# Optimization experiments

Measured on AMD Instinct MI355X. Metric: run time of the kernel, lower is better.

## Reference

```python
import jax, jax.numpy as jnp
import numpy as np

NT, NRV, NR = 100000, 200000, 300000  # tile / road_vertex / road node counts
E = 400000                             # edges per edge type
B, H, P, A = 64, 128, 64, 512          # graphs, hidden, player_state_dim, action_dim


def _gat(h_src, h_dst, src, dst, W, a_s, a_d, b, n_dst):
    # PyG GATConv, heads=1, shared lin for src/dst, no self loops (bipartite)
    hs = h_src @ W                      # [Ns, H]
    hd = h_dst @ W                      # [Nd, H]
    e = jax.nn.leaky_relu((hs @ a_s)[src] + (hd @ a_d)[dst], 0.2)  # [E]
    m = jax.ops.segment_max(e, dst, num_segments=n_dst)
    w = jnp.exp(e - m[dst])
    denom = jax.ops.segment_sum(w, dst, num_segments=n_dst)
    alpha = w / jnp.maximum(denom[dst], 1e-16)                      # segment softmax
    out = jax.ops.segment_sum(alpha[:, None] * hs[src], dst, num_segments=n_dst)
    return out + b


def _mean_pool(x, batch, nb):
    s = jax.ops.segment_sum(x, batch, num_segments=nb)
    c = jax.ops.segment_sum(jnp.ones((x.shape[0],), x.dtype), batch, num_segments=nb)
    return s / jnp.maximum(c, 1.0)[:, None]


def setup_inputs():
    ks = iter(jax.random.split(jax.random.key(0), 64))
    f32 = jnp.float32

    def lin(i, o):
        return (jax.random.normal(next(ks), (i, o), f32) / np.float32(np.sqrt(i)))

    d = {}
    d['x_tile'] = jax.random.normal(next(ks), (NT, 8), f32)
    d['x_rv'] = jax.random.normal(next(ks), (NRV, 13), f32)
    d['x_road'] = jax.random.normal(next(ks), (NR, 4), f32)
    d['x_player'] = jax.random.normal(next(ks), (B, P), f32)
    # node encoders
    d['enc_t_W'] = lin(8, H);  d['enc_t_b'] = jnp.zeros((H,), f32)
    d['enc_rv_W'] = lin(13, H); d['enc_rv_b'] = jnp.zeros((H,), f32)
    d['enc_r_W'] = lin(4, H);  d['enc_r_b'] = jnp.zeros((H,), f32)
    # six GAT convs
    for name in ['rv2t', 't2rv', 'r2rv', 'rv2r', 't2r', 'r2t']:
        d[name + '_W'] = lin(H, H)
        d[name + '_as'] = jax.random.normal(next(ks), (H,), f32) * 0.1
        d[name + '_ad'] = jax.random.normal(next(ks), (H,), f32) * 0.1
        d[name + '_b'] = jnp.zeros((H,), f32)
    # player MLP + output head (input: 3H pooled + H player)
    d['fc1_W'] = lin(P, H); d['fc1_b'] = jnp.zeros((H,), f32)
    d['fc2_W'] = lin(H, H); d['fc2_b'] = jnp.zeros((H,), f32)
    d['out_W'] = lin(4 * H, A); d['out_b'] = jnp.zeros((A,), f32)
    # edges (src bounded by source-type count, dst by dest-type count)
    ri = lambda n, hi: jax.random.randint(n, (E,), 0, hi, jnp.int32)
    d['e_rv2t_src'] = ri(next(ks), NRV); d['e_rv2t_dst'] = ri(next(ks), NT)
    d['e_t2rv_src'] = ri(next(ks), NT);  d['e_t2rv_dst'] = ri(next(ks), NRV)
    d['e_r2rv_src'] = ri(next(ks), NR);  d['e_r2rv_dst'] = ri(next(ks), NRV)
    d['e_rv2r_src'] = ri(next(ks), NRV); d['e_rv2r_dst'] = ri(next(ks), NR)
    d['e_t2r_src'] = ri(next(ks), NT);   d['e_t2r_dst'] = ri(next(ks), NR)
    d['e_r2t_src'] = ri(next(ks), NR);   d['e_r2t_dst'] = ri(next(ks), NT)
    # batch assignment per node type
    d['batch_tile'] = jnp.sort(jax.random.randint(next(ks), (NT,), 0, B, jnp.int32))
    d['batch_rv'] = jnp.sort(jax.random.randint(next(ks), (NRV,), 0, B, jnp.int32))
    d['batch_road'] = jnp.sort(jax.random.randint(next(ks), (NR,), 0, B, jnp.int32))
    return d


def reference(x_tile, x_rv, x_road, x_player,
              enc_t_W, enc_t_b, enc_rv_W, enc_rv_b, enc_r_W, enc_r_b,
              rv2t_W, rv2t_as, rv2t_ad, rv2t_b,
              t2rv_W, t2rv_as, t2rv_ad, t2rv_b,
              r2rv_W, r2rv_as, r2rv_ad, r2rv_b,
              rv2r_W, rv2r_as, rv2r_ad, rv2r_b,
              t2r_W, t2r_as, t2r_ad, t2r_b,
              r2t_W, r2t_as, r2t_ad, r2t_b,
              fc1_W, fc1_b, fc2_W, fc2_b, out_W, out_b,
              e_rv2t_src, e_rv2t_dst, e_t2rv_src, e_t2rv_dst,
              e_r2rv_src, e_r2rv_dst, e_rv2r_src, e_rv2r_dst,
              e_t2r_src, e_t2r_dst, e_r2t_src, e_r2t_dst,
              batch_tile, batch_rv, batch_road):
    # node encoders
    h_t = x_tile @ enc_t_W + enc_t_b
    h_rv = x_rv @ enc_rv_W + enc_rv_b
    h_r = x_road @ enc_r_W + enc_r_b
    # hetero GAT, aggr='sum' over edge types per destination node type
    o_t = (_gat(h_rv, h_t, e_rv2t_src, e_rv2t_dst, rv2t_W, rv2t_as, rv2t_ad, rv2t_b, NT)
           + _gat(h_r, h_t, e_r2t_src, e_r2t_dst, r2t_W, r2t_as, r2t_ad, r2t_b, NT))
    o_rv = (_gat(h_t, h_rv, e_t2rv_src, e_t2rv_dst, t2rv_W, t2rv_as, t2rv_ad, t2rv_b, NRV)
            + _gat(h_r, h_rv, e_r2rv_src, e_r2rv_dst, r2rv_W, r2rv_as, r2rv_ad, r2rv_b, NRV))
    o_r = (_gat(h_rv, h_r, e_rv2r_src, e_rv2r_dst, rv2r_W, rv2r_as, rv2r_ad, rv2r_b, NR)
           + _gat(h_t, h_r, e_t2r_src, e_t2r_dst, t2r_W, t2r_as, t2r_ad, t2r_b, NR))
    # global mean pool per node type, concat -> [B, 3H]
    x_all = jnp.concatenate([_mean_pool(o_t, batch_tile, B),
                             _mean_pool(o_rv, batch_rv, B),
                             _mean_pool(o_r, batch_road, B)], axis=1)
    # player branch
    p = jax.nn.relu(x_player @ fc1_W + fc1_b)
    p = jax.nn.relu(p @ fc2_W + fc2_b)
    x = jnp.concatenate([x_all, p], axis=1)  # [B, 4H]
    return x @ out_W + out_b                 # [B, A]
```

## Files before the change

### kernel.cpp

```cpp
#include <hip/hip_runtime.h>


constexpr int kNT = 100000, kNRV = 200000, kNR = 300000, kE = 400000;
constexpr int kTOTE = 6 * kE;
constexpr int kSLOT = 1088;
constexpr int kPSZ  = 6 * kSLOT;
constexpr int kNB   = 367;

constexpr long long OFF_C    = 0;
constexpr long long OFF_VS   = 13056;
constexpr long long OFF_VD   = 13176;
constexpr long long OFF_P    = 13296;
constexpr long long OFF_XCAT = 19824;
constexpr long long OFF_LS   = 52592;
constexpr long long OFF_LD   = 1252592;
constexpr long long OFF_PB   = 52592;
constexpr long long OFF_W16  = 2452592;
constexpr long long OFF_DR2  = 3652592;
constexpr long long OFF_XR   = 6052592;

__constant__ const int kLSB[6] = {0, 200000, 300000, 600000, 800000, 900000};
__constant__ const int kDRB[6] = {0, 100000, 300000, 500000, 800000, 1100000};
__constant__ const int kDLEN[6] = {100000, 200000, 200000, 300000, 300000, 100000};

__global__ __launch_bounds__(256) void precompute_kernel(
    const float* encW_t, const float* encb_t,
    const float* encW_rv, const float* encb_rv,
    const float* encW_r, const float* encb_r,
    const float* W0, const float* as0, const float* ad0,
    const float* W1, const float* as1, const float* ad1,
    const float* W2, const float* as2, const float* ad2,
    const float* W3, const float* as3, const float* ad3,
    const float* W4, const float* as4, const float* ad4,
    const float* W5, const float* as5, const float* ad5,
    float* Cws, float* vsw, float* vdw)
{
  const float* encW[3] = {encW_t, encW_rv, encW_r};
  const float* encb[3] = {encb_t, encb_rv, encb_r};
  const int    Ks[3]   = {8, 13, 4};
  const float* Wv[6]  = {W0, W1, W2, W3, W4, W5};
  const float* asv[6] = {as0, as1, as2, as3, as4, as5};
  const float* adv[6] = {ad0, ad1, ad2, ad3, ad4, ad5};
  const int srcT[6] = {1, 0, 2, 1, 0, 2};
  const int dstT[6] = {0, 1, 1, 2, 2, 0};

  __shared__ float Cl[2176];
  __shared__ float wv[128];

  int et = blockIdx.x;
  int tid = threadIdx.x;
  int st = srcT[et], dt = dstT[et];
  const float* eW = encW[st];
  const float* eB = encb[st];
  int K = Ks[st];
  const float* W = Wv[et];
  const float* a_s = asv[et];
  const float* a_d = adv[et];
  float* Cslot = Cws + et * 2176;

  for (int idx = tid; idx < (K + 1) * 128; idx += 256) {
    int r = idx >> 7, j = idx & 127;
    const float* row = (r < K) ? (eW + r * 128) : eB;
    float acc = 0.f;
    for (int m = 0; m < 128; ++m) acc += row[m] * W[m * 128 + j];
    int o = (r < K) ? (r * 128 + j) : (2048 + j);
    Cl[o] = acc;
    Cslot[o] = acc;
  }
  if (tid < 128) {
    float acc = 0.f;
    for (int j = 0; j < 128; ++j) acc += W[tid * 128 + j] * a_d[j];
    wv[tid] = acc;
  }
  __syncthreads();
  if (tid <= K) {
    const float* row = (tid < K) ? (Cl + tid * 128) : (Cl + 2048);
    float acc = 0.f;
    for (int j = 0; j < 128; ++j) acc += row[j] * a_s[j];
    vsw[et * 20 + (tid < K ? tid : 16)] = acc;
  }
  int KD = Ks[dt];
  if (tid >= 32 && tid <= 32 + KD) {
    int k = tid - 32;
    const float* row = (k < KD) ? (encW[dt] + k * 128) : encb[dt];
    float acc = 0.f;
    for (int m = 0; m < 128; ++m) acc += row[m] * wv[m];
    vdw[et * 20 + (k < KD ? k : 16)] = acc;
  }
}

template <int K, int RH>
__device__ __forceinline__ void prep_one(
    const float* __restrict__ xr, float bf,
    const float* __restrict__ vsA, const float* __restrict__ vsB,
    const float* __restrict__ vdA, const float* __restrict__ vdB,
    float* lsA, float* lsB, float* ldA, float* ldB,
    float2* dr2A, float2* dr2B, _Float16* xrec)
{
  float a0 = 0.f, a1 = 0.f, a2 = 0.f, a3 = 0.f;
#pragma unroll
  for (int k = 0; k < K; ++k) {
    float xv = xr[k];
    a0 += xv * vsA[k]; a1 += xv * vsB[k];
    a2 += xv * vdA[k]; a3 += xv * vdB[k];
    xrec[k] = (_Float16)xv;
  }
#pragma unroll
  for (int k = K; k < RH; ++k) xrec[k] = (_Float16)0.f;
  *lsA = a0 + vsA[16];
  *lsB = a1 + vsB[16];
  *ldA = a2 + vdA[16];
  *ldB = a3 + vdB[16];
  *dr2A = make_float2(0.f, bf);
  *dr2B = make_float2(0.f, bf);
}

__global__ __launch_bounds__(256) void prep_kernel(
    const float* __restrict__ x_t, const float* __restrict__ x_rv,
    const float* __restrict__ x_r,
    const int* __restrict__ bt, const int* __restrict__ brv,
    const int* __restrict__ br,
    const float* __restrict__ vsw, const float* __restrict__ vdw,
    float* __restrict__ LS, float* __restrict__ LD,
    float2* __restrict__ DR2, _Float16* __restrict__ XR)
{
  int n = blockIdx.x * 256 + threadIdx.x;
  if (n >= kNT + kNRV + kNR) return;
  if (n < kNT) {
    prep_one<8, 8>(x_t + n * 8, (float)bt[n],
                   vsw + 1 * 20, vsw + 4 * 20, vdw + 0 * 20, vdw + 5 * 20,
                   LS + 200000 + n, LS + 800000 + n,
                   LD + 0 + n, LD + 1100000 + n,
                   DR2 + 0 + n, DR2 + 1100000 + n,
                   XR + (long long)n * 8);
  } else if (n < kNT + kNRV) {
    int m = n - kNT;
    prep_one<13, 16>(x_rv + m * 13, (float)brv[m],
                     vsw + 0 * 20, vsw + 3 * 20, vdw + 1 * 20, vdw + 2 * 20,
                     LS + 0 + m, LS + 600000 + m,
                     LD + 100000 + m, LD + 300000 + m,
                     DR2 + 100000 + m, DR2 + 300000 + m,
                     XR + 800000 + (long long)m * 16);
  } else {
    int m = n - kNT - kNRV;
    prep_one<4, 4>(x_r + m * 4, (float)br[m],
                   vsw + 2 * 20, vsw + 5 * 20, vdw + 3 * 20, vdw + 4 * 20,
                   LS + 300000 + m, LS + 900000 + m,
                   LD + 500000 + m, LD + 800000 + m,
                   DR2 + 500000 + m, DR2 + 800000 + m,
                   XR + 4000000 + (long long)m * 4);
  }
}

__global__ __launch_bounds__(256) void passA_kernel(
    const int* s0, const int* s1, const int* s2,
    const int* s3, const int* s4, const int* s5,
    const int* d0, const int* d1, const int* d2,
    const int* d3, const int* d4, const int* d5,
    const float* __restrict__ LS, const float* __restrict__ LD,
    float* __restrict__ DR2f, _Float16* __restrict__ W16)
{
  int i = blockIdx.x * 256 + threadIdx.x;
  if (i >= kTOTE) return;
  int et = i / kE;
  int e = i - et * kE;
  const int* sp; const int* dp;
  switch (et) {
    case 0: sp = s0; dp = d0; break;
    case 1: sp = s1; dp = d1; break;
    case 2: sp = s2; dp = d2; break;
    case 3: sp = s3; dp = d3; break;
    case 4: sp = s4; dp = d4; break;
    default: sp = s5; dp = d5; break;
  }
  int lsb = kLSB[et], drb = kDRB[et];
  int s = sp[e], d = dp[e];
  float t = LS[lsb + s] + LD[drb + d];
  t = t > 0.f ? t : 0.2f * t;
  _Float16 h = (_Float16)__expf(t);
  W16[i] = h;
  unsafeAtomicAdd(&DR2f[(long long)(drb + d) * 2], (float)h);
}

template <int K, int RH>
__device__ __forceinline__ void passB_loop(
    const int* __restrict__ sp, const int* __restrict__ dp,
    int drb, int dlen, long long xrb,
    const _Float16* __restrict__ W16et, const float2* __restrict__ DR2,
    const _Float16* __restrict__ XR, float* __restrict__ lp,
    int start, int stride)
{
  int nItems = kE + dlen;
  for (int i = start; i < nItems; i += stride) {
    if (i < kE) {
      int s = sp[i], d = dp[i];
      float2 rec = DR2[drb + d];
      float w = (float)W16et[i];
      float alpha = w / fmaxf(rec.x, 1e-16f);
      int b = (int)rec.y;
      const _Float16* xp = XR + xrb + (long long)s * RH;
      float xv[K];
      if constexpr (RH == 4) {
        union { uint2 u; _Float16 h[4]; } U;
        U.u = *(const uint2*)xp;
#pragma unroll
        for (int k = 0; k < K; ++k) xv[k] = (float)U.h[k];
      } else if constexpr (RH == 8) {
        union { uint4 u; _Float16 h[8]; } U;
        U.u = *(const uint4*)xp;
#pragma unroll
        for (int k = 0; k < K; ++k) xv[k] = (float)U.h[k];
      } else {
        union { uint4 u[2]; _Float16 h[16]; } U;
        U.u[0] = *(const uint4*)xp;
        U.u[1] = *(const uint4*)(xp + 8);
#pragma unroll
        for (int k = 0; k < K; ++k) xv[k] = (float)U.h[k];
      }
#pragma unroll
      for (int k = 0; k < K; ++k) atomicAdd(lp + k * 64 + b, alpha * xv[k]);
    } else {
      int j = i - kE;
      float2 rec = DR2[drb + j];
      if (rec.x > 0.f) atomicAdd(lp + 1024 + (int)rec.y, 1.f);
    }
  }
}

__global__ __launch_bounds__(256) void passB_kernel(
    const int* s0, const int* s1, const int* s2,
    const int* s3, const int* s4, const int* s5,
    const int* d0, const int* d1, const int* d2,
    const int* d3, const int* d4, const int* d5,
    const _Float16* __restrict__ W16, const float2* __restrict__ DR2,
    const _Float16* __restrict__ XR, float* __restrict__ PB)
{
  __shared__ float lp[kSLOT];
  for (int j = threadIdx.x; j < kSLOT; j += 256) lp[j] = 0.f;
  __syncthreads();
  int et  = blockIdx.x / kNB;
  int blk = blockIdx.x - et * kNB;
  int start = blk * 256 + threadIdx.x;
  int stride = kNB * 256;
  int drb = kDRB[et], dlen = kDLEN[et];
  const _Float16* W16et = W16 + (long long)et * kE;
  switch (et) {
    case 0: passB_loop<13,16>(s0, d0, drb, dlen, 800000,  W16et, DR2, XR, lp, start, stride); break;
    case 1: passB_loop< 8, 8>(s1, d1, drb, dlen, 0,       W16et, DR2, XR, lp, start, stride); break;
    case 2: passB_loop< 4, 4>(s2, d2, drb, dlen, 4000000, W16et, DR2, XR, lp, start, stride); break;
    case 3: passB_loop<13,16>(s3, d3, drb, dlen, 800000,  W16et, DR2, XR, lp, start, stride); break;
    case 4: passB_loop< 8, 8>(s4, d4, drb, dlen, 0,       W16et, DR2, XR, lp, start, stride); break;
    default: passB_loop<4, 4>(s5, d5, drb, dlen, 4000000, W16et, DR2, XR, lp, start, stride); break;
  }
  __syncthreads();
  float* dst = PB + (long long)blockIdx.x * kSLOT;
  for (int j = threadIdx.x; j < kSLOT; j += 256) dst[j] = lp[j];
}

__global__ __launch_bounds__(256) void reduceP_kernel(
    const float* __restrict__ PB, float* __restrict__ P)
{
  int j = blockIdx.x * 256 + threadIdx.x;
  if (j >= kPSZ) return;
  int et = j / kSLOT;
  int jj = j - et * kSLOT;
  const float* base = PB + (long long)et * kNB * kSLOT + jj;
  float s = 0.f;
  int b = 0;
  for (; b + 8 <= kNB; b += 8) {
    float v0 = base[(long long)(b + 0) * kSLOT];
    float v1 = base[(long long)(b + 1) * kSLOT];
    float v2 = base[(long long)(b + 2) * kSLOT];
    float v3 = base[(long long)(b + 3) * kSLOT];
    float v4 = base[(long long)(b + 4) * kSLOT];
    float v5 = base[(long long)(b + 5) * kSLOT];
    float v6 = base[(long long)(b + 6) * kSLOT];
    float v7 = base[(long long)(b + 7) * kSLOT];
    s += ((v0 + v1) + (v2 + v3)) + ((v4 + v5) + (v6 + v7));
  }
  for (; b < kNB; ++b) s += base[(long long)b * kSLOT];
  P[j] = s;
}

__device__ __forceinline__ int lowb(const int* a, int n, int v) {
  int lo = 0, hi = n;
  while (lo < hi) { int mid = (lo + hi) >> 1; if (a[mid] < v) lo = mid + 1; else hi = mid; }
  return lo;
}

__global__ __launch_bounds__(128) void finalize_kernel(
    const int* __restrict__ bt, const int* __restrict__ brv, const int* __restrict__ br,
    const float* __restrict__ xp,
    const float* __restrict__ fc1W, const float* __restrict__ fc1b,
    const float* __restrict__ fc2W, const float* __restrict__ fc2b,
    const float* __restrict__ b_rv2t, const float* __restrict__ b_r2t,
    const float* __restrict__ b_t2rv, const float* __restrict__ b_r2rv,
    const float* __restrict__ b_rv2r, const float* __restrict__ b_t2r,
    const float* __restrict__ Cws, const float* __restrict__ P,
    float* __restrict__ xcat)
{
  int b = blockIdx.x, tid = threadIdx.x;
  __shared__ float xps[64];
  __shared__ float p1s[128];
  __shared__ int cnts[3];
  if (tid < 64) xps[tid] = xp[b * 64 + tid];
  if (tid < 3) {
    const int* ba = (tid == 0) ? bt : (tid == 1 ? brv : br);
    int N = (tid == 0) ? kNT : (tid == 1 ? kNRV : kNR);
    cnts[tid] = lowb(ba, N, b + 1) - lowb(ba, N, b);
  }
  __syncthreads();
  float a = fc1b[tid];
  for (int k = 0; k < 64; ++k) a += xps[k] * fc1W[k * 128 + tid];
  p1s[tid] = fmaxf(a, 0.f);
  __syncthreads();
  float a2 = fc2b[tid];
  for (int k = 0; k < 128; ++k) a2 += p1s[k] * fc2W[k * 128 + tid];
  xcat[b * 512 + 384 + tid] = fmaxf(a2, 0.f);
  const int etA[3] = {0, 1, 3}, etB[3] = {5, 2, 4};
  const int KAv[3] = {13, 8, 13}, KBv[3] = {4, 4, 8};
  for (int t3 = 0; t3 < 3; ++t3) {
    int eA = etA[t3], eB = etB[t3];
    const float* CA = Cws + eA * 2176;
    const float* CB = Cws + eB * 2176;
    const float* pA = P + eA * kSLOT;
    const float* pB = P + eB * kSLOT;
    float cA = pA[1024 + b];
    float cB = pB[1024 + b];
    float v = cA * CA[2048 + tid] + cB * CB[2048 + tid];
    for (int k = 0; k < KAv[t3]; ++k) v += pA[k * 64 + b] * CA[k * 128 + tid];
    for (int k = 0; k < KBv[t3]; ++k) v += pB[k * 64 + b] * CB[k * 128 + tid];
    float cnt = (float)max(cnts[t3], 1);
    const float* bb1 = (t3 == 0) ? b_rv2t : (t3 == 1 ? b_t2rv : b_rv2r);
    const float* bb2 = (t3 == 0) ? b_r2t  : (t3 == 1 ? b_r2rv : b_t2r);
    xcat[b * 512 + t3 * 128 + tid] = v / cnt + bb1[tid] + bb2[tid];
  }
}

__global__ __launch_bounds__(256) void out_kernel(
    const float* __restrict__ xcat, const float* __restrict__ outW,
    const float* __restrict__ outb, float* __restrict__ out)
{
  int g = blockIdx.x * 256 + threadIdx.x;
  int r = g >> 9, c = g & 511;
  const float* xr = xcat + r * 512;
  float acc = outb[c];
  for (int k = 0; k < 512; ++k) acc += xr[k] * outW[k * 512 + c];
  out[g] = acc;
}

extern "C" void kernel_launch(void* const* d_in, const int* in_sizes, int n_in,
                              void* d_out, int out_size, void* d_ws, size_t ws_size,
                              hipStream_t stream) {
  const float* x_tile   = (const float*)d_in[0];
  const float* x_rv     = (const float*)d_in[1];
  const float* x_road   = (const float*)d_in[2];
  const float* x_player = (const float*)d_in[3];
  const float* enc_t_W  = (const float*)d_in[4];
  const float* enc_t_b  = (const float*)d_in[5];
  const float* enc_rv_W = (const float*)d_in[6];
  const float* enc_rv_b = (const float*)d_in[7];
  const float* enc_r_W  = (const float*)d_in[8];
  const float* enc_r_b  = (const float*)d_in[9];
  const float* W[6]; const float* As[6]; const float* Ad[6]; const float* Bb[6];
  for (int et = 0; et < 6; ++et) {
    W[et]  = (const float*)d_in[10 + 4 * et];
    As[et] = (const float*)d_in[11 + 4 * et];
    Ad[et] = (const float*)d_in[12 + 4 * et];
    Bb[et] = (const float*)d_in[13 + 4 * et];
  }
  const float* fc1W = (const float*)d_in[34];
  const float* fc1b = (const float*)d_in[35];
  const float* fc2W = (const float*)d_in[36];
  const float* fc2b = (const float*)d_in[37];
  const float* outW = (const float*)d_in[38];
  const float* outb = (const float*)d_in[39];
  const int* esrc[6]; const int* edst[6];
  for (int et = 0; et < 6; ++et) {
    esrc[et] = (const int*)d_in[40 + 2 * et];
    edst[et] = (const int*)d_in[41 + 2 * et];
  }
  const int* batch_t  = (const int*)d_in[52];
  const int* batch_rv = (const int*)d_in[53];
  const int* batch_r  = (const int*)d_in[54];

  float* wsF = (float*)d_ws;
  float* Cws  = wsF + OFF_C;
  float* vsw  = wsF + OFF_VS;
  float* vdw  = wsF + OFF_VD;
  float* P    = wsF + OFF_P;
  float* xcat = wsF + OFF_XCAT;
  float* LS   = wsF + OFF_LS;
  float* LD   = wsF + OFF_LD;
  float* PB   = wsF + OFF_PB;
  _Float16* W16 = (_Float16*)(wsF + OFF_W16);
  float2* DR2 = (float2*)(wsF + OFF_DR2);
  float* DR2f = wsF + OFF_DR2;
  _Float16* XR = (_Float16*)(wsF + OFF_XR);
  float* out  = (float*)d_out;

  precompute_kernel<<<6, 256, 0, stream>>>(
      enc_t_W, enc_t_b, enc_rv_W, enc_rv_b, enc_r_W, enc_r_b,
      W[0], As[0], Ad[0], W[1], As[1], Ad[1], W[2], As[2], Ad[2],
      W[3], As[3], Ad[3], W[4], As[4], Ad[4], W[5], As[5], Ad[5],
      Cws, vsw, vdw);

  prep_kernel<<<(kNT + kNRV + kNR + 255) / 256, 256, 0, stream>>>(
      x_tile, x_rv, x_road, batch_t, batch_rv, batch_r, vsw, vdw,
      LS, LD, DR2, XR);

  passA_kernel<<<(kTOTE + 255) / 256, 256, 0, stream>>>(
      esrc[0], esrc[1], esrc[2], esrc[3], esrc[4], esrc[5],
      edst[0], edst[1], edst[2], edst[3], edst[4], edst[5],
      LS, LD, DR2f, W16);

  passB_kernel<<<6 * kNB, 256, 0, stream>>>(
      esrc[0], esrc[1], esrc[2], esrc[3], esrc[4], esrc[5],
      edst[0], edst[1], edst[2], edst[3], edst[4], edst[5],
      W16, DR2, XR, PB);

  reduceP_kernel<<<(kPSZ + 255) / 256, 256, 0, stream>>>(PB, P);

  finalize_kernel<<<64, 128, 0, stream>>>(
      batch_t, batch_rv, batch_r, x_player,
      fc1W, fc1b, fc2W, fc2b,
      Bb[0], Bb[5], Bb[1], Bb[2], Bb[3], Bb[4],
      Cws, P, xcat);

  out_kernel<<<128, 256, 0, stream>>>(xcat, outW, outb, out);

  (void)in_sizes; (void)n_in; (void)out_size; (void)ws_size;
}
```

Measured before the change: 515.9 us.

## Map edge types to XCDs via blockIdx modulo 8 for L2 locality

Both passA and passB now launch a fixed grid of 2048 blocks. Blocks are routed by blockIdx&7, which assumes round-robin dispatch across the 8 XCDs, so each XCD works on a contiguous edge range or a single edge type. This is meant to keep the gathered LS/LD/DR2/XR data for one edge type in that XCD's L2 instead of spreading it across all of them. The degree-count loop in passB now does a wave-level segmented scan, so runs of nodes in the same graph produce one shared-memory atomic instead of one each. reduceP is rewritten for the new per-block layout, and it relies on the block-to-XCD mapping being as assumed.

After: 537.8 us. +4.3%, slower.

```diff
diff --git a/kernel.cpp b/kernel.cpp
--- a/kernel.cpp
+++ b/kernel.cpp
@@ -5,7 +5,7 @@
 constexpr int kTOTE = 6 * kE;
 constexpr int kSLOT = 1088;
 constexpr int kPSZ  = 6 * kSLOT;
-constexpr int kNB   = 367;
+constexpr int kGRID = 2048;
 
 constexpr long long OFF_C    = 0;
 constexpr long long OFF_VS   = 13056;
@@ -22,6 +22,12 @@
 __constant__ const int kLSB[6] = {0, 200000, 300000, 600000, 800000, 900000};
 __constant__ const int kDRB[6] = {0, 100000, 300000, 500000, 800000, 1100000};
 __constant__ const int kDLEN[6] = {100000, 200000, 200000, 300000, 300000, 100000};
+
+__constant__ const int kXCD2ET[8] = {0, 0, 1, 2, 3, 3, 4, 5};
+__constant__ const int kXCDSUB[8] = {0, 1, 0, 0, 0, 1, 0, 0};
+__constant__ const int kETNX[6]   = {2, 1, 1, 2, 1, 1};
+__constant__ const int kETXCDA[6] = {0, 2, 3, 4, 6, 7};
+__constant__ const int kETXCDB[6] = {1, 2, 3, 5, 6, 7};
 
 __global__ __launch_bounds__(256) void precompute_kernel(
     const float* encW_t, const float* encb_t,
@@ -152,19 +158,14 @@
   }
 }
 
-__global__ __launch_bounds__(256) void passA_kernel(
+__device__ __forceinline__ void pickSD(
+    int et,
     const int* s0, const int* s1, const int* s2,
     const int* s3, const int* s4, const int* s5,
     const int* d0, const int* d1, const int* d2,
     const int* d3, const int* d4, const int* d5,
-    const float* __restrict__ LS, const float* __restrict__ LD,
-    float* __restrict__ DR2f, _Float16* __restrict__ W16)
-{
-  int i = blockIdx.x * 256 + threadIdx.x;
-  if (i >= kTOTE) return;
-  int et = i / kE;
-  int e = i - et * kE;
-  const int* sp; const int* dp;
+    const int*& sp, const int*& dp)
+{
   switch (et) {
     case 0: sp = s0; dp = d0; break;
     case 1: sp = s1; dp = d1; break;
@@ -173,13 +174,46 @@
     case 4: sp = s4; dp = d4; break;
     default: sp = s5; dp = d5; break;
   }
-  int lsb = kLSB[et], drb = kDRB[et];
-  int s = sp[e], d = dp[e];
-  float t = LS[lsb + s] + LD[drb + d];
-  t = t > 0.f ? t : 0.2f * t;
-  _Float16 h = (_Float16)__expf(t);
-  W16[i] = h;
-  unsafeAtomicAdd(&DR2f[(long long)(drb + d) * 2], (float)h);
+}
+
+__global__ __launch_bounds__(256, 8) void passA_kernel(
+    const int* s0, const int* s1, const int* s2,
+    const int* s3, const int* s4, const int* s5,
+    const int* d0, const int* d1, const int* d2,
+    const int* d3, const int* d4, const int* d5,
+    const float* __restrict__ LS, const float* __restrict__ LD,
+    float* __restrict__ DR2f, _Float16* __restrict__ W16)
+{
+  int xcd  = blockIdx.x & 7;
+  int slot = blockIdx.x >> 3;
+  int c0 = xcd * (kTOTE / 8);
+  int c1 = c0 + (kTOTE / 8);
+  int etA = c0 / kE;
+  int eA1 = (etA + 1) * kE;
+  if (eA1 > c1) eA1 = c1;
+
+  for (int half = 0; half < 2; ++half) {
+    int et, rs, re;
+    if (half == 0) {
+      et = etA; rs = c0; re = eA1;
+    } else {
+      if (eA1 >= c1) break;
+      et = etA + 1; rs = eA1; re = c1;
+    }
+    const int* sp; const int* dp;
+    pickSD(et, s0, s1, s2, s3, s4, s5, d0, d1, d2, d3, d4, d5, sp, dp);
+    int lsb = kLSB[et], drb = kDRB[et];
+    int ebase = et * kE;
+    for (int i = rs + slot * 256 + (int)threadIdx.x; i < re; i += 65536) {
+      int e = i - ebase;
+      int s = sp[e], d = dp[e];
+      float t = LS[lsb + s] + LD[drb + d];
+      t = t > 0.f ? t : 0.2f * t;
+      _Float16 h = (_Float16)__expf(t);
+      W16[i] = h;
+      unsafeAtomicAdd(&DR2f[(long long)(drb + d) * 2], (float)h);
+    }
+  }
 }
 
 template <int K, int RH>
@@ -188,46 +222,59 @@
     int drb, int dlen, long long xrb,
     const _Float16* __restrict__ W16et, const float2* __restrict__ DR2,
     const _Float16* __restrict__ XR, float* __restrict__ lp,
-    int start, int stride)
-{
-  int nItems = kE + dlen;
-  for (int i = start; i < nItems; i += stride) {
-    if (i < kE) {
-      int s = sp[i], d = dp[i];
-      float2 rec = DR2[drb + d];
-      float w = (float)W16et[i];
-      float alpha = w / fmaxf(rec.x, 1e-16f);
-      int b = (int)rec.y;
-      const _Float16* xp = XR + xrb + (long long)s * RH;
-      float xv[K];
-      if constexpr (RH == 4) {
-        union { uint2 u; _Float16 h[4]; } U;
-        U.u = *(const uint2*)xp;
-#pragma unroll
-        for (int k = 0; k < K; ++k) xv[k] = (float)U.h[k];
-      } else if constexpr (RH == 8) {
-        union { uint4 u; _Float16 h[8]; } U;
-        U.u = *(const uint4*)xp;
-#pragma unroll
-        for (int k = 0; k < K; ++k) xv[k] = (float)U.h[k];
-      } else {
-        union { uint4 u[2]; _Float16 h[16]; } U;
-        U.u[0] = *(const uint4*)xp;
-        U.u[1] = *(const uint4*)(xp + 8);
-#pragma unroll
-        for (int k = 0; k < K; ++k) xv[k] = (float)U.h[k];
-      }
-#pragma unroll
-      for (int k = 0; k < K; ++k) atomicAdd(lp + k * 64 + b, alpha * xv[k]);
+    int bIdx, int stride)
+{
+  int tid = threadIdx.x;
+  int lane = tid & 63;
+
+  for (int i = bIdx * 256 + tid; i < kE; i += stride) {
+    int s = sp[i], d = dp[i];
+    float2 rec = DR2[drb + d];
+    float w = (float)W16et[i];
+    float alpha = w / fmaxf(rec.x, 1e-16f);
+    int b = (int)rec.y;
+    const _Float16* xp = XR + xrb + (long long)s * RH;
+    float xv[K];
+    if constexpr (RH == 4) {
+      union { uint2 u; _Float16 h[4]; } U;
+      U.u = *(const uint2*)xp;
+#pragma unroll
+      for (int k = 0; k < K; ++k) xv[k] = (float)U.h[k];
+    } else if constexpr (RH == 8) {
+      union { uint4 u; _Float16 h[8]; } U;
+      U.u = *(const uint4*)xp;
+#pragma unroll
+      for (int k = 0; k < K; ++k) xv[k] = (float)U.h[k];
     } else {
-      int j = i - kE;
-      float2 rec = DR2[drb + j];
-      if (rec.x > 0.f) atomicAdd(lp + 1024 + (int)rec.y, 1.f);
+      union { uint4 u[2]; _Float16 h[16]; } U;
+      U.u[0] = *(const uint4*)xp;
+      U.u[1] = *(const uint4*)(xp + 8);
+#pragma unroll
+      for (int k = 0; k < K; ++k) xv[k] = (float)U.h[k];
     }
-  }
-}
-
-__global__ __launch_bounds__(256) void passB_kernel(
+#pragma unroll
+    for (int k = 0; k < K; ++k) atomicAdd(lp + k * 64 + b, alpha * xv[k]);
+  }
+
+  for (int base = bIdx * 256 + (tid & ~63); base < dlen; base += stride) {
+    int j = base + lane;
+    bool act = j < dlen;
+    float2 rec = act ? DR2[drb + j] : make_float2(0.f, 0.f);
+    int b = act ? (int)rec.y : (64 + lane);
+    int v = (act && rec.x > 0.f) ? 1 : 0;
+#pragma unroll
+    for (int d2 = 1; d2 < 64; d2 <<= 1) {
+      int ob = __shfl_up(b, d2);
+      int ov = __shfl_up(v, d2);
+      if (lane >= d2 && ob == b) v += ov;
+    }
+    int bn = __shfl_down(b, 1);
+    bool tailq = (lane == 63) || (bn != b);
+    if (tailq && v > 0) atomicAdd(lp + 1024 + b, (float)v);
+  }
+}
+
+__global__ __launch_bounds__(256, 8) void passB_kernel(
     const int* s0, const int* s1, const int* s2,
     const int* s3, const int* s4, const int* s5,
     const int* d0, const int* d1, const int* d2,
@@ -238,19 +285,21 @@
   __shared__ float lp[kSLOT];
   for (int j = threadIdx.x; j < kSLOT; j += 256) lp[j] = 0.f;
   __syncthreads();
-  int et  = blockIdx.x / kNB;
-  int blk = blockIdx.x - et * kNB;
-  int start = blk * 256 + threadIdx.x;
-  int stride = kNB * 256;
+  int xcd  = blockIdx.x & 7;
+  int slot = blockIdx.x >> 3;
+  int et = kXCD2ET[xcd];
+  int nx = kETNX[et];
+  int bIdx = slot * nx + kXCDSUB[xcd];
+  int stride = 65536 * nx;
   int drb = kDRB[et], dlen = kDLEN[et];
   const _Float16* W16et = W16 + (long long)et * kE;
   switch (et) {
-    case 0: passB_loop<13,16>(s0, d0, drb, dlen, 800000,  W16et, DR2, XR, lp, start, stride); break;
-    case 1: passB_loop< 8, 8>(s1, d1, drb, dlen, 0,       W16et, DR2, XR, lp, start, stride); break;
-    case 2: passB_loop< 4, 4>(s2, d2, drb, dlen, 4000000, W16et, DR2, XR, lp, start, stride); break;
-    case 3: passB_loop<13,16>(s3, d3, drb, dlen, 800000,  W16et, DR2, XR, lp, start, stride); break;
-    case 4: passB_loop< 8, 8>(s4, d4, drb, dlen, 0,       W16et, DR2, XR, lp, start, stride); break;
-    default: passB_loop<4, 4>(s5, d5, drb, dlen, 4000000, W16et, DR2, XR, lp, start, stride); break;
+    case 0: passB_loop<13,16>(s0, d0, drb, dlen, 800000,  W16et, DR2, XR, lp, bIdx, stride); break;
+    case 1: passB_loop< 8, 8>(s1, d1, drb, dlen, 0,       W16et, DR2, XR, lp, bIdx, stride); break;
+    case 2: passB_loop< 4, 4>(s2, d2, drb, dlen, 4000000, W16et, DR2, XR, lp, bIdx, stride); break;
+    case 3: passB_loop<13,16>(s3, d3, drb, dlen, 800000,  W16et, DR2, XR, lp, bIdx, stride); break;
+    case 4: passB_loop< 8, 8>(s4, d4, drb, dlen, 0,       W16et, DR2, XR, lp, bIdx, stride); break;
+    default: passB_loop<4, 4>(s5, d5, drb, dlen, 4000000, W16et, DR2, XR, lp, bIdx, stride); break;
   }
   __syncthreads();
   float* dst = PB + (long long)blockIdx.x * kSLOT;
@@ -264,21 +313,19 @@
   if (j >= kPSZ) return;
   int et = j / kSLOT;
   int jj = j - et * kSLOT;
-  const float* base = PB + (long long)et * kNB * kSLOT + jj;
   float s = 0.f;
-  int b = 0;
-  for (; b + 8 <= kNB; b += 8) {
-    float v0 = base[(long long)(b + 0) * kSLOT];
-    float v1 = base[(long long)(b + 1) * kSLOT];
-    float v2 = base[(long long)(b + 2) * kSLOT];
-    float v3 = base[(long long)(b + 3) * kSLOT];
-    float v4 = base[(long long)(b + 4) * kSLOT];
-    float v5 = base[(long long)(b + 5) * kSLOT];
-    float v6 = base[(long long)(b + 6) * kSLOT];
-    float v7 = base[(long long)(b + 7) * kSLOT];
-    s += ((v0 + v1) + (v2 + v3)) + ((v4 + v5) + (v6 + v7));
-  }
-  for (; b < kNB; ++b) s += base[(long long)b * kSLOT];
+  {
+    const float* base = PB + (long long)kETXCDA[et] * kSLOT + jj;
+#pragma unroll 8
+    for (int slot = 0; slot < 256; ++slot)
+      s += base[(long long)slot * (8 * kSLOT)];
+  }
+  if (kETNX[et] == 2) {
+    const float* base = PB + (long long)kETXCDB[et] * kSLOT + jj;
+#pragma unroll 8
+    for (int slot = 0; slot < 256; ++slot)
+      s += base[(long long)slot * (8 * kSLOT)];
+  }
   P[j] = s;
 }
 
@@ -409,12 +456,12 @@
       x_tile, x_rv, x_road, batch_t, batch_rv, batch_r, vsw, vdw,
       LS, LD, DR2, XR);
 
-  passA_kernel<<<(kTOTE + 255) / 256, 256, 0, stream>>>(
+  passA_kernel<<<kGRID, 256, 0, stream>>>(
       esrc[0], esrc[1], esrc[2], esrc[3], esrc[4], esrc[5],
       edst[0], edst[1], edst[2], edst[3], edst[4], edst[5],
       LS, LD, DR2f, W16);
 
-  passB_kernel<<<6 * kNB, 256, 0, stream>>>(
+  passB_kernel<<<kGRID, 256, 0, stream>>>(
       esrc[0], esrc[1], esrc[2], esrc[3], esrc[4], esrc[5],
       edst[0], edst[1], edst[2], edst[3], edst[4], edst[5],
       W16, DR2, XR, PB);
```

## Pack per-node features with logits, recompute edge weights, and reduce partials atomically

Applied to the files above, without the earlier changes.

Each source node now gets one packed record holding its fp16 features and its source-side attention logits, so a single vector load serves both. The destination logit and the graph id are packed into one float by storing the batch index in the low mantissa bits. The fp16 edge-weight buffer is dropped: edge weights are recomputed in the second pass instead of stored. Each thread handles five edges to raise memory-level parallelism. Node counts are reduced with a wave-level segmented scan, and per-block partial sums go into 8 slabs via atomics instead of a full per-block partial array. The trade-offs are extra exp work, slightly perturbed logits from the mantissa embedding, and atomic contention on the slabs.

After: 527.0 us. 2.1% more time.

```diff
diff --git a/kernel.cpp b/kernel.cpp
--- a/kernel.cpp
+++ b/kernel.cpp
@@ -2,26 +2,44 @@
 
 
 constexpr int kNT = 100000, kNRV = 200000, kNR = 300000, kE = 400000;
-constexpr int kTOTE = 6 * kE;
 constexpr int kSLOT = 1088;
 constexpr int kPSZ  = 6 * kSLOT;
-constexpr int kNB   = 367;
+constexpr int kNBE  = 342;
+constexpr int kNTH  = kNBE * 256;
+constexpr int kEPT  = 5;
 
 constexpr long long OFF_C    = 0;
 constexpr long long OFF_VS   = 13056;
 constexpr long long OFF_VD   = 13176;
 constexpr long long OFF_P    = 13296;
 constexpr long long OFF_XCAT = 19824;
-constexpr long long OFF_LS   = 52592;
-constexpr long long OFF_LD   = 1252592;
-constexpr long long OFF_PB   = 52592;
-constexpr long long OFF_W16  = 2452592;
-constexpr long long OFF_DR2  = 3652592;
-constexpr long long OFF_XR   = 6052592;
-
-__constant__ const int kLSB[6] = {0, 200000, 300000, 600000, 800000, 900000};
-__constant__ const int kDRB[6] = {0, 100000, 300000, 500000, 800000, 1100000};
-__constant__ const int kDLEN[6] = {100000, 200000, 200000, 300000, 300000, 100000};
+constexpr long long OFF_SRV  = 52592;
+constexpr long long OFF_ST   = 3252592;
+constexpr long long OFF_SR   = 4052592;
+constexpr long long OFF_LDD  = 5252592;
+constexpr long long OFF_P8   = 7652592;
+
+__constant__ const int kDRB[6]   = {0, 100000, 300000, 500000, 800000, 1100000};
+__constant__ const int kDLEN[6]  = {100000, 200000, 200000, 300000, 300000, 100000};
+__constant__ const int kLSOFF[6] = {7, 4, 2, 8, 5, 3};
+__constant__ const int kRSZ[6]   = {16, 8, 4, 16, 8, 4};
+
+__device__ __forceinline__ int lowb(const int* a, int n, int v) {
+  int lo = 0, hi = n;
+  while (lo < hi) { int mid = (lo + hi) >> 1; if (a[mid] < v) lo = mid + 1; else hi = mid; }
+  return lo;
+}
+
+static __device__ __forceinline__ unsigned p2h(float a, float b) {
+  _Float16 ha = (_Float16)a, hb = (_Float16)b;
+  unsigned short ua = __builtin_bit_cast(unsigned short, ha);
+  unsigned short ub = __builtin_bit_cast(unsigned short, hb);
+  return (unsigned)ua | ((unsigned)ub << 16);
+}
+
+static __device__ __forceinline__ float emb(float ld, int b) {
+  return __uint_as_float((__float_as_uint(ld) & ~63u) | (unsigned)b);
+}
 
 __global__ __launch_bounds__(256) void precompute_kernel(
     const float* encW_t, const float* encb_t,
@@ -33,7 +51,7 @@
     const float* W3, const float* as3, const float* ad3,
     const float* W4, const float* as4, const float* ad4,
     const float* W5, const float* as5, const float* ad5,
-    float* Cws, float* vsw, float* vdw)
+    float* Cws, float* vsw, float* vdw, float* P8)
 {
   const float* encW[3] = {encW_t, encW_rv, encW_r};
   const float* encb[3] = {encb_t, encb_rv, encb_r};
@@ -58,6 +76,10 @@
   const float* a_d = adv[et];
   float* Cslot = Cws + et * 2176;
 
+  for (int c = 0; c < 8; ++c)
+    for (int i = tid; i < kSLOT; i += 256)
+      P8[c * kPSZ + et * kSLOT + i] = 0.f;
+
   for (int idx = tid; idx < (K + 1) * 128; idx += 256) {
     int r = idx >> 7, j = idx & 127;
     const float* row = (r < K) ? (eW + r * 128) : eB;
@@ -89,82 +111,96 @@
   }
 }
 
-template <int K, int RH>
-__device__ __forceinline__ void prep_one(
-    const float* __restrict__ xr, float bf,
-    const float* __restrict__ vsA, const float* __restrict__ vsB,
-    const float* __restrict__ vdA, const float* __restrict__ vdB,
-    float* lsA, float* lsB, float* ldA, float* ldB,
-    float2* dr2A, float2* dr2B, _Float16* xrec)
-{
-  float a0 = 0.f, a1 = 0.f, a2 = 0.f, a3 = 0.f;
-#pragma unroll
-  for (int k = 0; k < K; ++k) {
-    float xv = xr[k];
-    a0 += xv * vsA[k]; a1 += xv * vsB[k];
-    a2 += xv * vdA[k]; a3 += xv * vdB[k];
-    xrec[k] = (_Float16)xv;
-  }
-#pragma unroll
-  for (int k = K; k < RH; ++k) xrec[k] = (_Float16)0.f;
-  *lsA = a0 + vsA[16];
-  *lsB = a1 + vsB[16];
-  *ldA = a2 + vdA[16];
-  *ldB = a3 + vdB[16];
-  *dr2A = make_float2(0.f, bf);
-  *dr2B = make_float2(0.f, bf);
-}
-
 __global__ __launch_bounds__(256) void prep_kernel(
     const float* __restrict__ x_t, const float* __restrict__ x_rv,
     const float* __restrict__ x_r,
     const int* __restrict__ bt, const int* __restrict__ brv,
     const int* __restrict__ br,
     const float* __restrict__ vsw, const float* __restrict__ vdw,
-    float* __restrict__ LS, float* __restrict__ LD,
-    float2* __restrict__ DR2, _Float16* __restrict__ XR)
+    uint4* __restrict__ SRVq, uint4* __restrict__ STq, uint4* __restrict__ SRq,
+    float* __restrict__ LDDf)
 {
   int n = blockIdx.x * 256 + threadIdx.x;
   if (n >= kNT + kNRV + kNR) return;
   if (n < kNT) {
-    prep_one<8, 8>(x_t + n * 8, (float)bt[n],
-                   vsw + 1 * 20, vsw + 4 * 20, vdw + 0 * 20, vdw + 5 * 20,
-                   LS + 200000 + n, LS + 800000 + n,
-                   LD + 0 + n, LD + 1100000 + n,
-                   DR2 + 0 + n, DR2 + 1100000 + n,
-                   XR + (long long)n * 8);
+    const float* xr = x_t + n * 8;
+    int b = bt[n];
+    const float* vsA = vsw + 1 * 20, *vsB = vsw + 4 * 20;
+    const float* vdA = vdw + 0 * 20, *vdB = vdw + 5 * 20;
+    float x[8]; float a0 = 0, a1 = 0, a2 = 0, a3 = 0;
+#pragma unroll
+    for (int k = 0; k < 8; ++k) {
+      x[k] = xr[k];
+      a0 += x[k] * vsA[k]; a1 += x[k] * vsB[k];
+      a2 += x[k] * vdA[k]; a3 += x[k] * vdB[k];
+    }
+    float ls1 = a0 + vsA[16], ls4 = a1 + vsB[16];
+    float ld0 = a2 + vdA[16], ld5 = a3 + vdB[16];
+    STq[(long long)n * 2] =
+        make_uint4(p2h(x[0], x[1]), p2h(x[2], x[3]), p2h(x[4], x[5]), p2h(x[6], x[7]));
+    STq[(long long)n * 2 + 1] =
+        make_uint4(__float_as_uint(ls1), __float_as_uint(ls4), 0, 0);
+    LDDf[(long long)n * 2] = emb(ld0, b);
+    LDDf[(long long)n * 2 + 1] = 0.f;
+    LDDf[(long long)(1100000 + n) * 2] = emb(ld5, b);
+    LDDf[(long long)(1100000 + n) * 2 + 1] = 0.f;
   } else if (n < kNT + kNRV) {
     int m = n - kNT;
-    prep_one<13, 16>(x_rv + m * 13, (float)brv[m],
-                     vsw + 0 * 20, vsw + 3 * 20, vdw + 1 * 20, vdw + 2 * 20,
-                     LS + 0 + m, LS + 600000 + m,
-                     LD + 100000 + m, LD + 300000 + m,
-                     DR2 + 100000 + m, DR2 + 300000 + m,
-                     XR + 800000 + (long long)m * 16);
+    const float* xr = x_rv + m * 13;
+    int b = brv[m];
+    const float* vsA = vsw + 0 * 20, *vsB = vsw + 3 * 20;
+    const float* vdA = vdw + 1 * 20, *vdB = vdw + 2 * 20;
+    float x[13]; float a0 = 0, a1 = 0, a2 = 0, a3 = 0;
+#pragma unroll
+    for (int k = 0; k < 13; ++k) {
+      x[k] = xr[k];
+      a0 += x[k] * vsA[k]; a1 += x[k] * vsB[k];
+      a2 += x[k] * vdA[k]; a3 += x[k] * vdB[k];
+    }
+    float ls0 = a0 + vsA[16], ls3 = a1 + vsB[16];
+    float ld1 = a2 + vdA[16], ld2 = a3 + vdB[16];
+    SRVq[(long long)m * 4] =
+        make_uint4(p2h(x[0], x[1]), p2h(x[2], x[3]), p2h(x[4], x[5]), p2h(x[6], x[7]));
+    SRVq[(long long)m * 4 + 1] =
+        make_uint4(p2h(x[8], x[9]), p2h(x[10], x[11]), p2h(x[12], 0.f),
+                   __float_as_uint(ls0));
+    SRVq[(long long)m * 4 + 2] = make_uint4(__float_as_uint(ls3), 0, 0, 0);
+    LDDf[(long long)(100000 + m) * 2] = emb(ld1, b);
+    LDDf[(long long)(100000 + m) * 2 + 1] = 0.f;
+    LDDf[(long long)(300000 + m) * 2] = emb(ld2, b);
+    LDDf[(long long)(300000 + m) * 2 + 1] = 0.f;
   } else {
     int m = n - kNT - kNRV;
-    prep_one<4, 4>(x_r + m * 4, (float)br[m],
-                   vsw + 2 * 20, vsw + 5 * 20, vdw + 3 * 20, vdw + 4 * 20,
-                   LS + 300000 + m, LS + 900000 + m,
-                   LD + 500000 + m, LD + 800000 + m,
-                   DR2 + 500000 + m, DR2 + 800000 + m,
-                   XR + 4000000 + (long long)m * 4);
-  }
-}
-
-__global__ __launch_bounds__(256) void passA_kernel(
+    const float* xr = x_r + m * 4;
+    int b = br[m];
+    const float* vsA = vsw + 2 * 20, *vsB = vsw + 5 * 20;
+    const float* vdA = vdw + 3 * 20, *vdB = vdw + 4 * 20;
+    float x[4]; float a0 = 0, a1 = 0, a2 = 0, a3 = 0;
+#pragma unroll
+    for (int k = 0; k < 4; ++k) {
+      x[k] = xr[k];
+      a0 += x[k] * vsA[k]; a1 += x[k] * vsB[k];
+      a2 += x[k] * vdA[k]; a3 += x[k] * vdB[k];
+    }
+    float ls2 = a0 + vsA[16], ls5 = a1 + vsB[16];
+    float ld3 = a2 + vdA[16], ld4 = a3 + vdB[16];
+    SRq[m] = make_uint4(p2h(x[0], x[1]), p2h(x[2], x[3]),
+                        __float_as_uint(ls2), __float_as_uint(ls5));
+    LDDf[(long long)(500000 + m) * 2] = emb(ld3, b);
+    LDDf[(long long)(500000 + m) * 2 + 1] = 0.f;
+    LDDf[(long long)(800000 + m) * 2] = emb(ld4, b);
+    LDDf[(long long)(800000 + m) * 2 + 1] = 0.f;
+  }
+}
+
+__device__ __forceinline__ void pickSD(
+    int et,
     const int* s0, const int* s1, const int* s2,
     const int* s3, const int* s4, const int* s5,
     const int* d0, const int* d1, const int* d2,
     const int* d3, const int* d4, const int* d5,
-    const float* __restrict__ LS, const float* __restrict__ LD,
-    float* __restrict__ DR2f, _Float16* __restrict__ W16)
-{
-  int i = blockIdx.x * 256 + threadIdx.x;
-  if (i >= kTOTE) return;
-  int et = i / kE;
-  int e = i - et * kE;
-  const int* sp; const int* dp;
+    const int*& sp, const int*& dp)
+{
   switch (et) {
     case 0: sp = s0; dp = d0; break;
     case 1: sp = s1; dp = d1; break;
@@ -173,119 +209,181 @@
     case 4: sp = s4; dp = d4; break;
     default: sp = s5; dp = d5; break;
   }
-  int lsb = kLSB[et], drb = kDRB[et];
-  int s = sp[e], d = dp[e];
-  float t = LS[lsb + s] + LD[drb + d];
-  t = t > 0.f ? t : 0.2f * t;
-  _Float16 h = (_Float16)__expf(t);
-  W16[i] = h;
-  unsafeAtomicAdd(&DR2f[(long long)(drb + d) * 2], (float)h);
-}
-
-template <int K, int RH>
-__device__ __forceinline__ void passB_loop(
-    const int* __restrict__ sp, const int* __restrict__ dp,
-    int drb, int dlen, long long xrb,
-    const _Float16* __restrict__ W16et, const float2* __restrict__ DR2,
-    const _Float16* __restrict__ XR, float* __restrict__ lp,
-    int start, int stride)
-{
-  int nItems = kE + dlen;
-  for (int i = start; i < nItems; i += stride) {
-    if (i < kE) {
-      int s = sp[i], d = dp[i];
-      float2 rec = DR2[drb + d];
-      float w = (float)W16et[i];
-      float alpha = w / fmaxf(rec.x, 1e-16f);
-      int b = (int)rec.y;
-      const _Float16* xp = XR + xrb + (long long)s * RH;
-      float xv[K];
-      if constexpr (RH == 4) {
-        union { uint2 u; _Float16 h[4]; } U;
-        U.u = *(const uint2*)xp;
-#pragma unroll
-        for (int k = 0; k < K; ++k) xv[k] = (float)U.h[k];
-      } else if constexpr (RH == 8) {
-        union { uint4 u; _Float16 h[8]; } U;
-        U.u = *(const uint4*)xp;
-#pragma unroll
-        for (int k = 0; k < K; ++k) xv[k] = (float)U.h[k];
-      } else {
-        union { uint4 u[2]; _Float16 h[16]; } U;
-        U.u[0] = *(const uint4*)xp;
-        U.u[1] = *(const uint4*)(xp + 8);
-#pragma unroll
-        for (int k = 0; k < K; ++k) xv[k] = (float)U.h[k];
-      }
-#pragma unroll
-      for (int k = 0; k < K; ++k) atomicAdd(lp + k * 64 + b, alpha * xv[k]);
-    } else {
-      int j = i - kE;
-      float2 rec = DR2[drb + j];
-      if (rec.x > 0.f) atomicAdd(lp + 1024 + (int)rec.y, 1.f);
-    }
-  }
-}
-
-__global__ __launch_bounds__(256) void passB_kernel(
+}
+
+__global__ __launch_bounds__(256, 8) void edgeA_kernel(
     const int* s0, const int* s1, const int* s2,
     const int* s3, const int* s4, const int* s5,
     const int* d0, const int* d1, const int* d2,
     const int* d3, const int* d4, const int* d5,
-    const _Float16* __restrict__ W16, const float2* __restrict__ DR2,
-    const _Float16* __restrict__ XR, float* __restrict__ PB)
+    const unsigned* __restrict__ SRVu, const unsigned* __restrict__ STu,
+    const unsigned* __restrict__ SRu, float* __restrict__ LDDf)
+{
+  int et = blockIdx.x / kNBE;
+  int bIdx = blockIdx.x - et * kNBE;
+  const int* sp; const int* dp;
+  pickSD(et, s0, s1, s2, s3, s4, s5, d0, d1, d2, d3, d4, d5, sp, dp);
+  const unsigned* su = (et == 1 || et == 4) ? STu : ((et == 2 || et == 5) ? SRu : SRVu);
+  const int rsz = kRSZ[et];
+  const int lso = kLSOFF[et];
+  const int drb = kDRB[et];
+  int base = bIdx * 256 + (int)threadIdx.x;
+
+  int s[kEPT], d[kEPT]; bool ok[kEPT];
+#pragma unroll
+  for (int j = 0; j < kEPT; ++j) {
+    int e = base + j * kNTH;
+    ok[j] = e < kE;
+    int ee = ok[j] ? e : 0;
+    s[j] = sp[ee]; d[j] = dp[ee];
+  }
+  float ls[kEPT];
+#pragma unroll
+  for (int j = 0; j < kEPT; ++j)
+    ls[j] = __uint_as_float(su[(long long)s[j] * rsz + lso]);
+  float ld[kEPT];
+#pragma unroll
+  for (int j = 0; j < kEPT; ++j)
+    ld[j] = LDDf[(long long)(drb + d[j]) * 2];
+#pragma unroll
+  for (int j = 0; j < kEPT; ++j) {
+    float t = ls[j] + ld[j];
+    t = t > 0.f ? t : 0.2f * t;
+    float w = __expf(t);
+    if (ok[j]) unsafeAtomicAdd(&LDDf[(long long)(drb + d[j]) * 2 + 1], w);
+  }
+}
+
+template <int TYPE, int RSEL>
+__device__ __forceinline__ void ebflow(
+    int bIdx,
+    const int* __restrict__ sp, const int* __restrict__ dp,
+    const uint4* __restrict__ srq, const float2* __restrict__ LDD2,
+    int drb, int dlen, float* lp)
+{
+  constexpr int K = (TYPE == 0) ? 8 : ((TYPE == 1) ? 13 : 4);
+  const int tid = threadIdx.x;
+  const int lane = tid & 63;
+  int base = bIdx * 256 + tid;
+
+  int s[kEPT], d[kEPT]; bool ok[kEPT];
+#pragma unroll
+  for (int j = 0; j < kEPT; ++j) {
+    int e = base + j * kNTH;
+    ok[j] = e < kE;
+    int ee = ok[j] ? e : 0;
+    s[j] = sp[ee]; d[j] = dp[ee];
+  }
+  uint4 q0[kEPT], q1[kEPT];
+  float lsx[kEPT];
+#pragma unroll
+  for (int j = 0; j < kEPT; ++j) {
+    if (TYPE == 0) {
+      q0[j] = srq[(long long)s[j] * 2];
+      lsx[j] = __uint_as_float(
+          ((const unsigned*)srq)[(long long)s[j] * 8 + (RSEL ? 5 : 4)]);
+    } else if (TYPE == 1) {
+      q0[j] = srq[(long long)s[j] * 4];
+      q1[j] = srq[(long long)s[j] * 4 + 1];
+      lsx[j] = RSEL
+          ? __uint_as_float(((const unsigned*)srq)[(long long)s[j] * 16 + 8])
+          : __uint_as_float(q1[j].w);
+    } else {
+      q0[j] = srq[s[j]];
+      lsx[j] = __uint_as_float(RSEL ? q0[j].w : q0[j].z);
+    }
+  }
+  float2 f2[kEPT];
+#pragma unroll
+  for (int j = 0; j < kEPT; ++j) f2[j] = LDD2[drb + d[j]];
+
+#pragma unroll
+  for (int j = 0; j < kEPT; ++j) {
+    if (!ok[j]) continue;
+    int b = (int)(__float_as_uint(f2[j].x) & 63u);
+    float t = lsx[j] + f2[j].x;
+    t = t > 0.f ? t : 0.2f * t;
+    float w = __expf(t);
+    float alpha = w / fmaxf(f2[j].y, 1e-16f);
+    float xv[K];
+    if (TYPE == 0) {
+      const _Float16* h = (const _Float16*)&q0[j];
+#pragma unroll
+      for (int k = 0; k < 8; ++k) xv[k] = (float)h[k];
+    } else if (TYPE == 1) {
+      const _Float16* h = (const _Float16*)&q0[j];
+#pragma unroll
+      for (int k = 0; k < 8; ++k) xv[k] = (float)h[k];
+      const _Float16* h2 = (const _Float16*)&q1[j];
+#pragma unroll
+      for (int k = 0; k < 5; ++k) xv[8 + k] = (float)h2[k];
+    } else {
+      const _Float16* h = (const _Float16*)&q0[j];
+#pragma unroll
+      for (int k = 0; k < 4; ++k) xv[k] = (float)h[k];
+    }
+#pragma unroll
+    for (int k = 0; k < K; ++k) atomicAdd(lp + k * 64 + b, alpha * xv[k]);
+  }
+
+  for (int base2 = bIdx * 256 + (tid & ~63); base2 < dlen; base2 += kNTH) {
+    int j2 = base2 + lane;
+    bool a2 = j2 < dlen;
+    float2 r2 = a2 ? LDD2[drb + j2] : make_float2(0.f, 0.f);
+    int b2 = a2 ? (int)(__float_as_uint(r2.x) & 63u) : (64 + lane);
+    int v = (a2 && r2.y > 0.f) ? 1 : 0;
+#pragma unroll
+    for (int d2 = 1; d2 < 64; d2 <<= 1) {
+      int ob = __shfl_up(b2, d2);
+      int ov = __shfl_up(v, d2);
+      if (lane >= d2 && ob == b2) v += ov;
+    }
+    int bn = __shfl_down(b2, 1);
+    if (((lane == 63) || (bn != b2)) && v > 0) atomicAdd(lp + 1024 + b2, (float)v);
+  }
+}
+
+__global__ __launch_bounds__(256, 4) void edgeB_kernel(
+    const int* s0, const int* s1, const int* s2,
+    const int* s3, const int* s4, const int* s5,
+    const int* d0, const int* d1, const int* d2,
+    const int* d3, const int* d4, const int* d5,
+    const uint4* SRVq, const uint4* STq, const uint4* SRq,
+    const float2* __restrict__ LDD2, float* __restrict__ P8)
 {
   __shared__ float lp[kSLOT];
   for (int j = threadIdx.x; j < kSLOT; j += 256) lp[j] = 0.f;
   __syncthreads();
-  int et  = blockIdx.x / kNB;
-  int blk = blockIdx.x - et * kNB;
-  int start = blk * 256 + threadIdx.x;
-  int stride = kNB * 256;
-  int drb = kDRB[et], dlen = kDLEN[et];
-  const _Float16* W16et = W16 + (long long)et * kE;
+  int et = blockIdx.x / kNBE;
+  int bIdx = blockIdx.x - et * kNBE;
+  constexpr int KK[6] = {13, 8, 4, 13, 8, 4};
   switch (et) {
-    case 0: passB_loop<13,16>(s0, d0, drb, dlen, 800000,  W16et, DR2, XR, lp, start, stride); break;
-    case 1: passB_loop< 8, 8>(s1, d1, drb, dlen, 0,       W16et, DR2, XR, lp, start, stride); break;
-    case 2: passB_loop< 4, 4>(s2, d2, drb, dlen, 4000000, W16et, DR2, XR, lp, start, stride); break;
-    case 3: passB_loop<13,16>(s3, d3, drb, dlen, 800000,  W16et, DR2, XR, lp, start, stride); break;
-    case 4: passB_loop< 8, 8>(s4, d4, drb, dlen, 0,       W16et, DR2, XR, lp, start, stride); break;
-    default: passB_loop<4, 4>(s5, d5, drb, dlen, 4000000, W16et, DR2, XR, lp, start, stride); break;
+    case 0: ebflow<1, 0>(bIdx, s0, d0, SRVq, LDD2, 0,       100000, lp); break;
+    case 1: ebflow<0, 0>(bIdx, s1, d1, STq,  LDD2, 100000,  200000, lp); break;
+    case 2: ebflow<2, 0>(bIdx, s2, d2, SRq,  LDD2, 300000,  200000, lp); break;
+    case 3: ebflow<1, 1>(bIdx, s3, d3, SRVq, LDD2, 500000,  300000, lp); break;
+    case 4: ebflow<0, 1>(bIdx, s4, d4, STq,  LDD2, 800000,  300000, lp); break;
+    default: ebflow<2, 1>(bIdx, s5, d5, SRq, LDD2, 1100000, 100000, lp); break;
   }
   __syncthreads();
-  float* dst = PB + (long long)blockIdx.x * kSLOT;
-  for (int j = threadIdx.x; j < kSLOT; j += 256) dst[j] = lp[j];
-}
-
-__global__ __launch_bounds__(256) void reduceP_kernel(
-    const float* __restrict__ PB, float* __restrict__ P)
+  int K = KK[et];
+  float* slab = P8 + (long long)(blockIdx.x & 7) * kPSZ + (long long)et * kSLOT;
+  for (int i = threadIdx.x; i < kSLOT; i += 256) {
+    if (i >= K * 64 && i < 1024) continue;
+    float v = lp[i];
+    if (v != 0.f) unsafeAtomicAdd(&slab[i], v);
+  }
+}
+
+__global__ __launch_bounds__(256) void reduceP8_kernel(
+    const float* __restrict__ P8, float* __restrict__ P)
 {
   int j = blockIdx.x * 256 + threadIdx.x;
   if (j >= kPSZ) return;
-  int et = j / kSLOT;
-  int jj = j - et * kSLOT;
-  const float* base = PB + (long long)et * kNB * kSLOT + jj;
   float s = 0.f;
-  int b = 0;
-  for (; b + 8 <= kNB; b += 8) {
-    float v0 = base[(long long)(b + 0) * kSLOT];
-    float v1 = base[(long long)(b + 1) * kSLOT];
-    float v2 = base[(long long)(b + 2) * kSLOT];
-    float v3 = base[(long long)(b + 3) * kSLOT];
-    float v4 = base[(long long)(b + 4) * kSLOT];
-    float v5 = base[(long long)(b + 5) * kSLOT];
-    float v6 = base[(long long)(b + 6) * kSLOT];
-    float v7 = base[(long long)(b + 7) * kSLOT];
-    s += ((v0 + v1) + (v2 + v3)) + ((v4 + v5) + (v6 + v7));
-  }
-  for (; b < kNB; ++b) s += base[(long long)b * kSLOT];
+#pragma unroll
+  for (int c = 0; c < 8; ++c) s += P8[c * kPSZ + j];
   P[j] = s;
-}
-
-__device__ __forceinline__ int lowb(const int* a, int n, int v) {
-  int lo = 0, hi = n;
-  while (lo < hi) { int mid = (lo + hi) >> 1; if (a[mid] < v) lo = mid + 1; else hi = mid; }
-  return lo;
 }
 
 __global__ __launch_bounds__(128) void finalize_kernel(
@@ -390,36 +488,35 @@
   float* vdw  = wsF + OFF_VD;
   float* P    = wsF + OFF_P;
   float* xcat = wsF + OFF_XCAT;
-  float* LS   = wsF + OFF_LS;
-  float* LD   = wsF + OFF_LD;
-  float* PB   = wsF + OFF_PB;
-  _Float16* W16 = (_Float16*)(wsF + OFF_W16);
-  float2* DR2 = (float2*)(wsF + OFF_DR2);
-  float* DR2f = wsF + OFF_DR2;
-  _Float16* XR = (_Float16*)(wsF + OFF_XR);
+  uint4* SRVq = (uint4*)(wsF + OFF_SRV);
+  uint4* STq  = (uint4*)(wsF + OFF_ST);
+  uint4* SRq  = (uint4*)(wsF + OFF_SR);
+  float* LDDf = wsF + OFF_LDD;
+  float2* LDD2 = (float2*)(wsF + OFF_LDD);
+  float* P8   = wsF + OFF_P8;
   float* out  = (float*)d_out;
 
   precompute_kernel<<<6, 256, 0, stream>>>(
       enc_t_W, enc_t_b, enc_rv_W, enc_rv_b, enc_r_W, enc_r_b,
       W[0], As[0], Ad[0], W[1], As[1], Ad[1], W[2], As[2], Ad[2],
       W[3], As[3], Ad[3], W[4], As[4], Ad[4], W[5], As[5], Ad[5],
-      Cws, vsw, vdw);
+      Cws, vsw, vdw, P8);
 
   prep_kernel<<<(kNT + kNRV + kNR + 255) / 256, 256, 0, stream>>>(
       x_tile, x_rv, x_road, batch_t, batch_rv, batch_r, vsw, vdw,
-      LS, LD, DR2, XR);
-
-  passA_kernel<<<(kTOTE + 255) / 256, 256, 0, stream>>>(
+      SRVq, STq, SRq, LDDf);
+
+  edgeA_kernel<<<6 * kNBE, 256, 0, stream>>>(
       esrc[0], esrc[1], esrc[2], esrc[3], esrc[4], esrc[5],
       edst[0], edst[1], edst[2], edst[3], edst[4], edst[5],
-      LS, LD, DR2f, W16);
-
-  passB_kernel<<<6 * kNB, 256, 0, stream>>>(
+      (const unsigned*)SRVq, (const unsigned*)STq, (const unsigned*)SRq, LDDf);
+
+  edgeB_kernel<<<6 * kNBE, 256, 0, stream>>>(
       esrc[0], esrc[1], esrc[2], esrc[3], esrc[4], esrc[5],
       edst[0], edst[1], edst[2], edst[3], edst[4], edst[5],
-      W16, DR2, XR, PB);
-
-  reduceP_kernel<<<(kPSZ + 255) / 256, 256, 0, stream>>>(PB, P);
+      SRVq, STq, SRq, LDD2, P8);
+
+  reduceP8_kernel<<<(kPSZ + 255) / 256, 256, 0, stream>>>(P8, P);
 
   finalize_kernel<<<64, 128, 0, stream>>>(
       batch_t, batch_rv, batch_r, x_player,
```
